# Performance work log

Hardware: AMD Instinct MI355X
Metric: run time of the kernel (lower is better)

The kernel has to match this reference:

```python
import jax, jax.numpy as jnp
import numpy as np

B, T, D = 8, 2048, 128        # batch, time, input_dim
C, CD = 8192, 128             # codebook_size, codebook_dim
COMMIT_W = 1.0                # commitment_weight
IN2Q_W = 0.25                 # input_to_quantize_commit_loss_weight
EPS = 1e-12


def setup_inputs() -> dict:
    key = jax.random.key(0)
    k = jax.random.split(key, 4)
    z = jax.random.normal(k[0], (B, T, D), jnp.float32)
    frozen_codebook = jax.random.normal(k[1], (C, CD), jnp.float32) * CD ** -0.5
    conv_v = jax.random.normal(k[2], (D, CD), jnp.float32) * CD ** -0.5  # weight-norm direction (1x1 conv weight squeezed)
    conv_g = jnp.linalg.norm(conv_v, axis=1)                             # weight-norm gain (torch init: g = ||v||)
    conv_b = jnp.zeros((D,), jnp.float32)
    return {"z": z, "frozen_codebook": frozen_codebook, "conv_v": conv_v,
            "conv_g": conv_g, "conv_b": conv_b}


def _implicit_codebook(fc, v, g, b):
    # weight-normed 1x1 conv == linear: w = g * v / ||v||_row ; out = fc @ w.T + b
    w = g[:, None] * v / jnp.linalg.norm(v, axis=1, keepdims=True)
    return fc @ w.T + b  # (C, D)


def _rotate_to(src, tgt):
    # rotation trick (Fifty et al.): Householder-style rotation, grads flow only through src
    sg = jax.lax.stop_gradient
    norm_src = jnp.linalg.norm(src, axis=-1, keepdims=True)
    norm_tgt = jnp.linalg.norm(tgt, axis=-1, keepdims=True)
    u = sg(src / jnp.maximum(norm_src, EPS))
    q = sg(tgt / jnp.maximum(norm_tgt, EPS))
    w = u + q
    w = sg(w / jnp.maximum(jnp.linalg.norm(w, axis=-1, keepdims=True), EPS))
    e = src
    rotated = (e
               - 2.0 * jnp.sum(e * w, -1, keepdims=True) * w
               + 2.0 * jnp.sum(e * u, -1, keepdims=True) * q)
    scale = sg(norm_tgt / jnp.maximum(norm_src, EPS))
    return rotated * scale


def reference(z, frozen_codebook, conv_v, conv_g, conv_b):
    sg = jax.lax.stop_gradient
    cb = _implicit_codebook(frozen_codebook, conv_v, conv_g, conv_b)  # (C, D)
    # squared euclidean distances -> same argmin as torch.cdist (p=2)
    d2 = (jnp.sum(z * z, -1, keepdims=True)
          - 2.0 * jnp.einsum('btd,cd->btc', z, cb)
          + jnp.sum(cb * cb, -1))                                     # (B, T, C)
    indices = jnp.argmin(d2, axis=-1)                                 # (B, T)
    z_q = cb[indices]                                                 # (B, T, D)
    commit = (jnp.mean((sg(z) - z_q) ** 2)
              + IN2Q_W * jnp.mean((z - sg(z_q)) ** 2))
    z_q = _rotate_to(z, z_q)
    return z_q, indices, commit * COMMIT_W
```

## Files before the change

### kernel.cpp

```cpp
#include <hip/hip_runtime.h>
#include <math.h>

#define NROWS 16384
#define DIM 128
#define NCODE 8192
#define EPSF 1e-12f

typedef float f32x4 __attribute__((ext_vector_type(4)));
typedef __bf16 bf16x8 __attribute__((ext_vector_type(8)));
typedef unsigned short u16x8 __attribute__((ext_vector_type(8)));

#define WS_NEED_BYTES 31571968ull

#define KT 12
#define TILEA 4096
#define TILEB 8192
#define KPB 3
#define CHUNK (TILEA + TILEB)

__device__ __forceinline__ float wave_sum(float x) {
#pragma unroll
  for (int off = 32; off > 0; off >>= 1) x += __shfl_xor(x, off, 64);
  return x;
}

__device__ __forceinline__ unsigned short f2bf(float x) {
  union { float f; unsigned int u; } v;
  v.f = x;
  unsigned int r = v.u + 0x7fffu + ((v.u >> 16) & 1u);
  return (unsigned short)(r >> 16);
}
__device__ __forceinline__ float bf2f(unsigned short h) {
  union { float f; unsigned int u; } v;
  v.u = ((unsigned int)h) << 16;
  return v.f;
}

__device__ __forceinline__ void gload_lds16(const unsigned short* g,
                                            unsigned short* l) {
  __builtin_amdgcn_global_load_lds(
      (const __attribute__((address_space(1))) void*)g,
      (__attribute__((address_space(3))) void*)l, 16, 0, 0);
}

__global__ __launch_bounds__(256) void wz_kernel(
    const float* __restrict__ z, const float* __restrict__ v,
    const float* __restrict__ g, unsigned short* __restrict__ zcat,
    float* __restrict__ Wt) {
  const int b = blockIdx.x;
  if (b < 3072) {
    const int id = b * 256 + threadIdx.x;
    const int row = id / 48, s = id - row * 48;
    const int kt = s >> 2, s4 = s & 3;
    const int seg = kt >> 2;
    const int d0 = ((kt & 3) << 5) + (s4 << 3);
    const int r = row & 127, rt = row >> 7;
    const int slotsw = s4 ^ ((r >> 1) & 3);

    const float* zp = &z[(size_t)row * DIM + d0];
    u16x8 out;
#pragma unroll
    for (int i = 0; i < 8; ++i) {
      const float x = zp[i];
      unsigned short bb = f2bf(x);
      if (seg == 2) bb = f2bf(x - bf2f(bb));
      out[i] = bb;
    }
    *(u16x8*)&zcat[(size_t)(rt * KT + kt) * TILEA + (r << 5) +
                   (slotsw << 3)] = out;
  } else {
    const int tid = threadIdx.x;
    const int wid = tid >> 6, lane = tid & 63;
    const int d = (b - 3072) * 4 + wid;
    const float v0 = v[d * DIM + lane], v1 = v[d * DIM + lane + 64];
    const float ss = wave_sum(fmaf(v0, v0, v1 * v1));
    const float sc = g[d] / sqrtf(ss);
    Wt[lane * DIM + d] = v0 * sc;
    Wt[(lane + 64) * DIM + d] = v1 * sc;
  }
}

__global__ __launch_bounds__(256, 2) void codebook_kernel(
    const float* __restrict__ fc, const float* __restrict__ Wt,
    const float* __restrict__ bias, float* __restrict__ cb,
    float* __restrict__ cnorm2, unsigned short* __restrict__ cbcat) {
  __shared__ float Ws[DIM][DIM];
  const int tid = threadIdx.x;
  for (int i = tid; i < 4096; i += 256)
    *(float4*)&Ws[0][i << 2] = *(const float4*)&Wt[i << 2];
  __syncthreads();

  const int lane = tid & 63, wid = tid >> 6;
  const int c0 = blockIdx.x * 16 + wid * 4;
  const float b0 = bias[lane], b1 = bias[lane + 64];

  for (int cc = 0; cc < 4; ++cc) {
    const int c = __builtin_amdgcn_readfirstlane(c0 + cc);
    float a0 = 0.f, a1 = 0.f;
    for (int k = 0; k < DIM; k += 4) {
      const float4 f4 = *(const float4*)&fc[c * DIM + k];
      a0 = fmaf(f4.x, Ws[k][lane], a0);
      a1 = fmaf(f4.x, Ws[k][lane + 64], a1);
      a0 = fmaf(f4.y, Ws[k + 1][lane], a0);
      a1 = fmaf(f4.y, Ws[k + 1][lane + 64], a1);
      a0 = fmaf(f4.z, Ws[k + 2][lane], a0);
      a1 = fmaf(f4.z, Ws[k + 2][lane + 64], a1);
      a0 = fmaf(f4.w, Ws[k + 3][lane], a0);
      a1 = fmaf(f4.w, Ws[k + 3][lane + 64], a1);
    }
    const float o0 = a0 + b0, o1 = a1 + b1;
    cb[c * DIM + lane] = o0;
    cb[c * DIM + lane + 64] = o1;
    const float ss = wave_sum(fmaf(o0, o0, o1 * o1));
    if (lane == 0) cnorm2[c] = ss;

    if (cbcat != nullptr) {
      const int ct = c >> 8, r = c & 255;
      const unsigned int swz = ((r >> 1) & 3) << 3;
      unsigned short* base = cbcat + (size_t)ct * (KT * TILEB);
#pragma unroll
      for (int h = 0; h < 2; ++h) {
        const int d = lane + 64 * h;
        const float val = h ? o1 : o0;
        const unsigned short hiv = f2bf(val);
        const unsigned short lov = f2bf(val - bf2f(hiv));
        const int ktl = d >> 5;
        const int off = (r << 5) + ((d & 31) ^ swz);
        base[ktl * TILEB + off] = hiv;
        base[(4 + ktl) * TILEB + off] = lov;
        base[(8 + ktl) * TILEB + off] = hiv;
      }
    }
  }
}

__global__ __launch_bounds__(256, 2) void mfma_argmin_kernel(
    const unsigned short* __restrict__ zcat,
    const unsigned short* __restrict__ cbcat,
    const float* __restrict__ cnorm2, float* __restrict__ pval,
    int* __restrict__ pidx) {
  __shared__ __align__(16) unsigned short S[KPB * CHUNK];

  const int xcd = blockIdx.x & 7, idx = blockIdx.x >> 3;
  const int rt = xcd * 16 + (idx & 15);
  const int ct = idx >> 4;

  const int tid = threadIdx.x;
  const int lane = tid & 63, wid = tid >> 6;
  const int wr = wid >> 1, wc = wid & 1;
  const int l15 = lane & 15, lg = lane >> 4;
  const int tid8 = tid * 8;

  const unsigned short* Ag = zcat + (size_t)rt * (KT * TILEA);
  const unsigned short* Bg = cbcat + (size_t)ct * (KT * TILEB);

  f32x4 acc[4][8];
#pragma unroll
  for (int mi = 0; mi < 4; ++mi)
#pragma unroll
    for (int ni = 0; ni < 8; ++ni) acc[mi][ni] = f32x4{0.f, 0.f, 0.f, 0.f};

  int aoff[4], boff[8];
#pragma unroll
  for (int i = 0; i < 4; ++i) {
    const int ra = wr * 64 + i * 16 + l15;
    aoff[i] = (ra << 5) + ((lg ^ ((ra >> 1) & 3)) << 3);
  }
#pragma unroll
  for (int i = 0; i < 8; ++i) {
    const int rc = wc * 128 + i * 16 + l15;
    boff[i] = TILEA + (rc << 5) + ((lg ^ ((rc >> 1) & 3)) << 3);
  }

  for (int it = 0; it < KT / KPB; ++it) {
    __syncthreads();
#pragma unroll
    for (int kk = 0; kk < KPB; ++kk) {
      const int kt = it * KPB + kk;
      const unsigned short* ag = Ag + kt * TILEA;
      const unsigned short* bg = Bg + kt * TILEB;
      unsigned short* la = &S[kk * CHUNK];
      unsigned short* lb = &S[kk * CHUNK + TILEA];
#pragma unroll
      for (int j = 0; j < 2; ++j)
        gload_lds16(ag + j * 2048 + tid8, la + j * 2048 + tid8);
#pragma unroll
      for (int j = 0; j < 4; ++j)
        gload_lds16(bg + j * 2048 + tid8, lb + j * 2048 + tid8);
    }
    __syncthreads();

#pragma unroll
    for (int kk = 0; kk < KPB; ++kk) {
      const int sb = kk * CHUNK;
      bf16x8 af[4], bfr[8];
#pragma unroll
      for (int i = 0; i < 4; ++i) af[i] = *(const bf16x8*)&S[sb + aoff[i]];
#pragma unroll
      for (int i = 0; i < 8; ++i) bfr[i] = *(const bf16x8*)&S[sb + boff[i]];
#pragma unroll
      for (int mi = 0; mi < 4; ++mi)
#pragma unroll
        for (int ni = 0; ni < 8; ++ni)
          acc[mi][ni] = __builtin_amdgcn_mfma_f32_16x16x32_bf16(
              af[mi], bfr[ni], acc[mi][ni], 0, 0, 0);
    }
  }
  __syncthreads();

  float* exv = (float*)&S[0];
  int* exi = (int*)&S[2048];

  float cn[8];
#pragma unroll
  for (int ni = 0; ni < 8; ++ni)
    cn[ni] = cnorm2[ct * 256 + wc * 128 + ni * 16 + l15];

#pragma unroll
  for (int mi = 0; mi < 4; ++mi) {
#pragma unroll
    for (int rg = 0; rg < 4; ++rg) {
      float bv = 3.4e38f;
      int bi = 0;
#pragma unroll
      for (int ni = 0; ni < 8; ++ni) {
        const float d = fmaf(-2.f, acc[mi][ni][rg], cn[ni]);
        if (d < bv) { bv = d; bi = ct * 256 + wc * 128 + ni * 16 + l15; }
      }
#pragma unroll
      for (int off = 1; off < 16; off <<= 1) {
        const float ov = __shfl_xor(bv, off, 64);
        const int oi = __shfl_xor(bi, off, 64);
        if (ov < bv || (ov == bv && oi < bi)) { bv = ov; bi = oi; }
      }
      if (l15 == 0) {
        const int rloc = wr * 64 + mi * 16 + (lg << 2) + rg;
        exv[wc * 128 + rloc] = bv;
        exi[wc * 128 + rloc] = bi;
      }
    }
  }
  __syncthreads();
  if (tid < 128) {
    float bv = exv[tid];
    int bi = exi[tid];
    const float v1 = exv[128 + tid];
    if (v1 < bv) { bv = v1; bi = exi[128 + tid]; }
    const int row = rt * 128 + tid;
    pval[(size_t)ct * NROWS + row] = bv;
    pidx[(size_t)ct * NROWS + row] = bi;
  }
}

__global__ void wprep_kernel(const float* __restrict__ v,
                             const float* __restrict__ g,
                             float* __restrict__ Wt) {
  const int d = blockIdx.x;
  const int lane = threadIdx.x;
  const float v0 = v[d * DIM + lane], v1 = v[d * DIM + lane + 64];
  const float ss = wave_sum(fmaf(v0, v0, v1 * v1));
  const float sc = g[d] / sqrtf(ss);
  Wt[lane * DIM + d] = v0 * sc;
  Wt[(lane + 64) * DIM + d] = v1 * sc;
}

__global__ __launch_bounds__(256, 1) void argmin_kernel(
    const float* __restrict__ z, const float* __restrict__ cb,
    const float* __restrict__ cnorm2, float* __restrict__ pval,
    int* __restrict__ pidx) {
  __shared__ float zs[128][DIM];
  __shared__ float cs[128][DIM];

  const int tid = threadIdx.x;
  const int rb = blockIdx.x >> 1;
  const int ch = blockIdx.x & 1;
  const int row0 = rb * 128;
  const int code0 = ch * (NCODE / 2);

  for (int i = tid; i < 128 * 32; i += 256) {
    const int r = i >> 5, f = i & 31;
    *(float4*)&zs[r][f << 2] = *(const float4*)&z[(row0 + r) * DIM + (f << 2)];
  }

  const int tx = tid & 15, ty = tid >> 4;
  const int sw = tx & 7;

  float best[8];
  int besti[8];
#pragma unroll
  for (int r = 0; r < 8; ++r) { best[r] = 3.4e38f; besti[r] = 0; }

  for (int cc = 0; cc < NCODE / 2; cc += 128) {
    __syncthreads();
    for (int i = tid; i < 128 * 32; i += 256) {
      const int r = i >> 5, f = i & 31;
      const int fg = f ^ (r & 7);
      *(float4*)&cs[r][f << 2] =
          *(const float4*)&cb[(code0 + cc + r) * DIM + (fg << 2)];
    }
    __syncthreads();

    float acc[8][8];
#pragma unroll
    for (int r = 0; r < 8; ++r)
#pragma unroll
      for (int j = 0; j < 8; ++j) acc[r][j] = 0.f;

    for (int k = 0; k < DIM; k += 4) {
      const int f = k >> 2;
      float4 zr[8], cr[8];
#pragma unroll
      for (int r = 0; r < 8; ++r) zr[r] = *(const float4*)&zs[ty + 16 * r][k];
      const int col = ((f ^ sw) << 2);
#pragma unroll
      for (int j = 0; j < 8; ++j) cr[j] = *(const float4*)&cs[tx + 16 * j][col];
#pragma unroll
      for (int r = 0; r < 8; ++r)
#pragma unroll
        for (int j = 0; j < 8; ++j) {
          acc[r][j] = fmaf(zr[r].x, cr[j].x, acc[r][j]);
          acc[r][j] = fmaf(zr[r].y, cr[j].y, acc[r][j]);
          acc[r][j] = fmaf(zr[r].z, cr[j].z, acc[r][j]);
          acc[r][j] = fmaf(zr[r].w, cr[j].w, acc[r][j]);
        }
    }

#pragma unroll
    for (int j = 0; j < 8; ++j) {
      const int code = code0 + cc + tx + 16 * j;
      const float cnv = cnorm2[code];
#pragma unroll
      for (int r = 0; r < 8; ++r) {
        const float s = fmaf(-2.f, acc[r][j], cnv);
        if (s < best[r]) { best[r] = s; besti[r] = code; }
      }
    }
  }

#pragma unroll
  for (int off = 1; off < 16; off <<= 1) {
#pragma unroll
    for (int r = 0; r < 8; ++r) {
      const float ov = __shfl_xor(best[r], off, 64);
      const int oi = __shfl_xor(besti[r], off, 64);
      if (ov < best[r] || (ov == best[r] && oi < besti[r])) {
        best[r] = ov;
        besti[r] = oi;
      }
    }
  }
  if (tx == 0) {
#pragma unroll
    for (int r = 0; r < 8; ++r) {
      const int row = row0 + ty + 16 * r;
      pval[(size_t)ch * NROWS + row] = best[r];
      pidx[(size_t)ch * NROWS + row] = besti[r];
    }
  }
}

__global__ __launch_bounds__(256) void rotate_kernel(
    const float* __restrict__ z, const float* __restrict__ cb,
    const float* __restrict__ pval, const int* __restrict__ pidx, int ntiles,
    float* __restrict__ out_zq, float* __restrict__ out_idx,
    float* __restrict__ partials) {
  const int tid = threadIdx.x;
  const int wid = tid >> 6, lane = tid & 63;
  const int row = blockIdx.x * 4 + wid;

  float bv = 3.4e38f;
  int bi = 0x7fffffff;
  if (lane < ntiles) {
    bv = pval[(size_t)lane * NROWS + row];
    bi = pidx[(size_t)lane * NROWS + row];
  }
#pragma unroll
  for (int off = 32; off > 0; off >>= 1) {
    const float ov = __shfl_xor(bv, off, 64);
    const int oi = __shfl_xor(bi, off, 64);
    if (ov < bv || (ov == bv && oi < bi)) { bv = ov; bi = oi; }
  }
  const int ci = bi;

  const float z0 = z[row * DIM + lane], z1 = z[row * DIM + lane + 64];
  const float c0 = cb[ci * DIM + lane], c1 = cb[ci * DIM + lane + 64];

  const float ns2 = wave_sum(fmaf(z0, z0, z1 * z1));
  const float nt2 = wave_sum(fmaf(c0, c0, c1 * c1));
  const float ns = sqrtf(ns2), nt = sqrtf(nt2);
  const float dns = fmaxf(ns, EPSF), dnt = fmaxf(nt, EPSF);
  const float u0 = z0 / dns, u1 = z1 / dns;
  const float q0 = c0 / dnt, q1 = c1 / dnt;
  float w0 = u0 + q0, w1 = u1 + q1;
  const float nw = sqrtf(wave_sum(fmaf(w0, w0, w1 * w1)));
  const float dnw = fmaxf(nw, EPSF);
  w0 /= dnw;
  w1 /= dnw;
  const float ew = wave_sum(fmaf(z0, w0, z1 * w1));
  const float eu = wave_sum(fmaf(z0, u0, z1 * u1));
  const float sc = nt / dns;
  const float o0 = (z0 - 2.f * ew * w0 + 2.f * eu * q0) * sc;
  const float o1 = (z1 - 2.f * ew * w1 + 2.f * eu * q1) * sc;
  out_zq[row * DIM + lane] = o0;
  out_zq[row * DIM + lane + 64] = o1;
  if (lane == 0) out_idx[row] = (float)ci;

  const float d0 = z0 - c0, d1 = z1 - c1;
  const float rsum = wave_sum(fmaf(d0, d0, d1 * d1));
  __shared__ float pr[4];
  if (lane == 0) pr[wid] = rsum;
  __syncthreads();
  if (tid == 0) partials[blockIdx.x] = (pr[0] + pr[1]) + (pr[2] + pr[3]);
}

__global__ void finalize_kernel(const float* __restrict__ partials,
                                float* __restrict__ out_commit) {
  __shared__ float red[256];
  const int tid = threadIdx.x;
  float s = 0.f;
  for (int i = tid; i < 4096; i += 256) s += partials[i];
  red[tid] = s;
  __syncthreads();
  for (int off = 128; off > 0; off >>= 1) {
    if (tid < off) red[tid] += red[tid + off];
    __syncthreads();
  }
  if (tid == 0) out_commit[0] = red[0] * (1.25f / ((float)NROWS * (float)DIM));
}

extern "C" void kernel_launch(void* const* d_in, const int* in_sizes, int n_in,
                              void* d_out, int out_size, void* d_ws,
                              size_t ws_size, hipStream_t stream) {
  const float* z = (const float*)d_in[0];
  const float* fc = (const float*)d_in[1];
  const float* conv_v = (const float*)d_in[2];
  const float* conv_g = (const float*)d_in[3];
  const float* conv_b = (const float*)d_in[4];
  float* out = (float*)d_out;

  float* ws = (float*)d_ws;
  float* cb = ws;
  float* cnorm2 = ws + 1048576;
  float* Wt = ws + 1056768;

  if (ws_size >= WS_NEED_BYTES) {
    unsigned short* zcat = (unsigned short*)(ws + 1073152);
    unsigned short* cbcat = (unsigned short*)(ws + 4218880);
    float* pval = ws + 5791744;
    int* pidx = (int*)(ws + 6840320);
    float* partials = ws + 7888896;

    wz_kernel<<<3104, 256, 0, stream>>>(z, conv_v, conv_g, zcat, Wt);
    codebook_kernel<<<NCODE / 16, 256, 0, stream>>>(fc, Wt, conv_b, cb, cnorm2,
                                                    cbcat);
    mfma_argmin_kernel<<<4096, 256, 0, stream>>>(zcat, cbcat, cnorm2, pval,
                                                 pidx);
    rotate_kernel<<<NROWS / 4, 256, 0, stream>>>(z, cb, pval, pidx, 32, out,
                                                 out + 2097152, partials);
    finalize_kernel<<<1, 256, 0, stream>>>(partials, out + 2113536);
  } else {
    float* pval = ws + 1073152;
    int* pidx = (int*)(ws + 1105920);
    float* partials = ws + 1138688;

    wprep_kernel<<<DIM, 64, 0, stream>>>(conv_v, conv_g, Wt);
    codebook_kernel<<<NCODE / 16, 256, 0, stream>>>(fc, Wt, conv_b, cb, cnorm2,
                                                    nullptr);
    argmin_kernel<<<256, 256, 0, stream>>>(z, cb, cnorm2, pval, pidx);
    rotate_kernel<<<NROWS / 4, 256, 0, stream>>>(z, cb, pval, pidx, 2, out,
                                                 out + 2097152, partials);
    finalize_kernel<<<1, 256, 0, stream>>>(partials, out + 2113536);
  }
}
```

Before: 201.5 us.

## Raise MFMA argmin occupancy and batch rotate rows per block

The MFMA argmin kernel now stages two K-chunks per barrier instead of three, which shrinks shared memory, and asks for three blocks per CU. B fragments are loaded one at a time inside the N loop to lower register pressure. The rotate step moves to a new kernel that handles 16 rows per block, giving fewer blocks and fewer partial sums for finalize to reduce. The tradeoff is more barriers per K sweep and less load batching, in exchange for higher occupancy.

Measured after the change: 221.6 us. +10.0%, slower.

```diff
diff --git a/kernel.cpp b/kernel.cpp
--- a/kernel.cpp
+++ b/kernel.cpp
@@ -15,7 +15,7 @@
 #define KT 12
 #define TILEA 4096
 #define TILEB 8192
-#define KPB 3
+#define KPB 2
 #define CHUNK (TILEA + TILEB)
 
 __device__ __forceinline__ float wave_sum(float x) {
@@ -134,7 +134,7 @@
   }
 }
 
-__global__ __launch_bounds__(256, 2) void mfma_argmin_kernel(
+__global__ __launch_bounds__(256, 3) void mfma_argmin_kernel(
     const unsigned short* __restrict__ zcat,
     const unsigned short* __restrict__ cbcat,
     const float* __restrict__ cnorm2, float* __restrict__ pval,
@@ -193,17 +193,17 @@
 #pragma unroll
     for (int kk = 0; kk < KPB; ++kk) {
       const int sb = kk * CHUNK;
-      bf16x8 af[4], bfr[8];
+      bf16x8 af[4];
 #pragma unroll
       for (int i = 0; i < 4; ++i) af[i] = *(const bf16x8*)&S[sb + aoff[i]];
 #pragma unroll
-      for (int i = 0; i < 8; ++i) bfr[i] = *(const bf16x8*)&S[sb + boff[i]];
-#pragma unroll
-      for (int mi = 0; mi < 4; ++mi)
-#pragma unroll
-        for (int ni = 0; ni < 8; ++ni)
+      for (int ni = 0; ni < 8; ++ni) {
+        const bf16x8 bfr = *(const bf16x8*)&S[sb + boff[ni]];
+#pragma unroll
+        for (int mi = 0; mi < 4; ++mi)
           acc[mi][ni] = __builtin_amdgcn_mfma_f32_16x16x32_bf16(
-              af[mi], bfr[ni], acc[mi][ni], 0, 0, 0);
+              af[mi], bfr, acc[mi][ni], 0, 0, 0);
+      }
     }
   }
   __syncthreads();
@@ -359,29 +359,11 @@
   }
 }
 
-__global__ __launch_bounds__(256) void rotate_kernel(
-    const float* __restrict__ z, const float* __restrict__ cb,
-    const float* __restrict__ pval, const int* __restrict__ pidx, int ntiles,
-    float* __restrict__ out_zq, float* __restrict__ out_idx,
-    float* __restrict__ partials) {
-  const int tid = threadIdx.x;
-  const int wid = tid >> 6, lane = tid & 63;
-  const int row = blockIdx.x * 4 + wid;
-
-  float bv = 3.4e38f;
-  int bi = 0x7fffffff;
-  if (lane < ntiles) {
-    bv = pval[(size_t)lane * NROWS + row];
-    bi = pidx[(size_t)lane * NROWS + row];
-  }
-#pragma unroll
-  for (int off = 32; off > 0; off >>= 1) {
-    const float ov = __shfl_xor(bv, off, 64);
-    const int oi = __shfl_xor(bi, off, 64);
-    if (ov < bv || (ov == bv && oi < bi)) { bv = ov; bi = oi; }
-  }
-  const int ci = bi;
-
+__device__ __forceinline__ float rotate_row(const float* __restrict__ z,
+                                            const float* __restrict__ cb,
+                                            int row, int ci, int lane,
+                                            float* __restrict__ out_zq,
+                                            float* __restrict__ out_idx) {
   const float z0 = z[row * DIM + lane], z1 = z[row * DIM + lane + 64];
   const float c0 = cb[ci * DIM + lane], c1 = cb[ci * DIM + lane + 64];
 
@@ -406,19 +388,74 @@
   if (lane == 0) out_idx[row] = (float)ci;
 
   const float d0 = z0 - c0, d1 = z1 - c1;
-  const float rsum = wave_sum(fmaf(d0, d0, d1 * d1));
+  return wave_sum(fmaf(d0, d0, d1 * d1));
+}
+
+__global__ __launch_bounds__(256) void rotate16_kernel(
+    const float* __restrict__ z, const float* __restrict__ cb,
+    const float* __restrict__ pval, const int* __restrict__ pidx,
+    float* __restrict__ out_zq, float* __restrict__ out_idx,
+    float* __restrict__ partials) {
+  const int tid = threadIdx.x;
+  const int wid = tid >> 6, lane = tid & 63;
+  float acc = 0.f;
+#pragma unroll
+  for (int j = 0; j < 4; ++j) {
+    const int row = blockIdx.x * 16 + wid * 4 + j;
+    float bv = 3.4e38f;
+    int bi = 0x7fffffff;
+    if (lane < 32) {
+      bv = pval[(size_t)lane * NROWS + row];
+      bi = pidx[(size_t)lane * NROWS + row];
+    }
+#pragma unroll
+    for (int off = 32; off > 0; off >>= 1) {
+      const float ov = __shfl_xor(bv, off, 64);
+      const int oi = __shfl_xor(bi, off, 64);
+      if (ov < bv || (ov == bv && oi < bi)) { bv = ov; bi = oi; }
+    }
+    acc += rotate_row(z, cb, row, bi, lane, out_zq, out_idx);
+  }
+  __shared__ float pr[4];
+  if (lane == 0) pr[wid] = acc;
+  __syncthreads();
+  if (tid == 0) partials[blockIdx.x] = (pr[0] + pr[1]) + (pr[2] + pr[3]);
+}
+
+__global__ __launch_bounds__(256) void rotate_kernel(
+    const float* __restrict__ z, const float* __restrict__ cb,
+    const float* __restrict__ pval, const int* __restrict__ pidx, int ntiles,
+    float* __restrict__ out_zq, float* __restrict__ out_idx,
+    float* __restrict__ partials) {
+  const int tid = threadIdx.x;
+  const int wid = tid >> 6, lane = tid & 63;
+  const int row = blockIdx.x * 4 + wid;
+
+  float bv = 3.4e38f;
+  int bi = 0x7fffffff;
+  if (lane < ntiles) {
+    bv = pval[(size_t)lane * NROWS + row];
+    bi = pidx[(size_t)lane * NROWS + row];
+  }
+#pragma unroll
+  for (int off = 32; off > 0; off >>= 1) {
+    const float ov = __shfl_xor(bv, off, 64);
+    const int oi = __shfl_xor(bi, off, 64);
+    if (ov < bv || (ov == bv && oi < bi)) { bv = ov; bi = oi; }
+  }
+  const float rsum = rotate_row(z, cb, row, bi, lane, out_zq, out_idx);
   __shared__ float pr[4];
   if (lane == 0) pr[wid] = rsum;
   __syncthreads();
   if (tid == 0) partials[blockIdx.x] = (pr[0] + pr[1]) + (pr[2] + pr[3]);
 }
 
-__global__ void finalize_kernel(const float* __restrict__ partials,
+__global__ void finalize_kernel(const float* __restrict__ partials, int n,
                                 float* __restrict__ out_commit) {
   __shared__ float red[256];
   const int tid = threadIdx.x;
   float s = 0.f;
-  for (int i = tid; i < 4096; i += 256) s += partials[i];
+  for (int i = tid; i < n; i += 256) s += partials[i];
   red[tid] = s;
   __syncthreads();
   for (int off = 128; off > 0; off >>= 1) {
@@ -455,9 +492,10 @@
                                                     cbcat);
     mfma_argmin_kernel<<<4096, 256, 0, stream>>>(zcat, cbcat, cnorm2, pval,
                                                  pidx);
-    rotate_kernel<<<NROWS / 4, 256, 0, stream>>>(z, cb, pval, pidx, 32, out,
-                                                 out + 2097152, partials);
-    finalize_kernel<<<1, 256, 0, stream>>>(partials, out + 2113536);
+    rotate16_kernel<<<NROWS / 16, 256, 0, stream>>>(z, cb, pval, pidx, out,
+                                                    out + 2097152, partials);
+    finalize_kernel<<<1, 256, 0, stream>>>(partials, NROWS / 16,
+                                           out + 2113536);
   } else {
     float* pval = ws + 1073152;
     int* pidx = (int*)(ws + 1105920);
@@ -469,6 +507,7 @@
     argmin_kernel<<<256, 256, 0, stream>>>(z, cb, cnorm2, pval, pidx);
     rotate_kernel<<<NROWS / 4, 256, 0, stream>>>(z, cb, pval, pidx, 2, out,
                                                  out + 2097152, partials);
-    finalize_kernel<<<1, 256, 0, stream>>>(partials, out + 2113536);
-  }
-}
+    finalize_kernel<<<1, 256, 0, stream>>>(partials, NROWS / 4,
+                                           out + 2113536);
+  }
+}
```
